# Performance work log

Hardware: AMD Instinct MI355X
Metric: run time of the kernel (lower is better)

## Reference

```python
import jax, jax.numpy as jnp
import numpy as np

B, Hn, Wn, C, NH, WS, SR = 4, 64, 64, 256, 8, 3, 8
HD = C // NH
N = Hn * Wn
L = WS * WS
PH, PW = Hn // SR, Wn // SR
P = PH * PW
T = 4096  # cpb table length
NEG = -1e30

def _l2norm(x, axis=-1):
    return x / jnp.maximum(jnp.linalg.norm(x, axis=axis, keepdims=True), 1e-12)

def _unfold(x, ws):
    # x: (B, C, H, W) -> (B, C, ws*ws, H*W), torch F.unfold channel ordering (C major)
    p = ws // 2
    b, c, h, w = x.shape
    xp = jnp.pad(x, ((0, 0), (0, 0), (p, p), (p, p)))
    pats = jnp.stack([xp[:, :, i:i + h, j:j + w] for i in range(ws) for j in range(ws)], axis=2)
    return pats.reshape(b, c, ws * ws, h * w)

def setup_inputs():
    key = jax.random.key(0)
    ks = jax.random.split(key, 16)
    def w(k, shape, s=0.02):
        return jax.random.normal(k, shape, jnp.float32) * s
    # buffers derived from the window geometry (get_seqlen_and_mask)
    ones = np.ones((Hn, Wn), np.float32)
    pad = WS // 2
    op = np.pad(ones, pad)
    pats = np.stack([op[i:i + Hn, j:j + Wn] for i in range(WS) for j in range(WS)], -1).reshape(N, L)
    padding_mask = jnp.asarray(pats == 0)
    seq_length_scale = jnp.asarray(np.log(pats.sum(-1, keepdims=True) + P).astype(np.float32))
    temperature = jnp.log(jnp.expm1(jnp.ones((NH, 1, 1), jnp.float32) / 0.24))
    return dict(
        x=jax.random.normal(ks[0], (B, N, C), jnp.float32),
        relative_pos_index=jax.random.randint(ks[1], (N, P), 0, T),
        relative_coords_table=jax.random.uniform(ks[2], (T, 2), jnp.float32, -1.0, 1.0),
        q_w=w(ks[3], (C, C)), q_b=jnp.zeros((C,), jnp.float32),
        kv_w=w(ks[4], (2 * C, C)), kv_b=jnp.zeros((2 * C,), jnp.float32),
        temperature=temperature,
        query_embedding=w(ks[5], (NH, 1, HD)),
        proj_w=w(ks[6], (C, C)), proj_b=jnp.zeros((C,), jnp.float32),
        sr_w=w(ks[7], (C, C)), sr_b=jnp.zeros((C,), jnp.float32),
        norm_g=jnp.ones((C,), jnp.float32), norm_b=jnp.zeros((C,), jnp.float32),
        cpb1_w=w(ks[8], (512, 2)), cpb1_b=jnp.zeros((512,), jnp.float32),
        cpb2_w=w(ks[9], (NH, 512)), cpb2_b=jnp.zeros((NH,), jnp.float32),
        rpb_local=w(ks[10], (NH, L), 0.0004),
        learnable_tokens=w(ks[11], (NH, HD, L)),
        learnable_bias=jnp.zeros((NH, 1, L), jnp.float32),
        seq_length_scale=seq_length_scale,
        padding_mask=padding_mask,
        H=Hn, W=Wn,
    )

def _forward(x, q_w, q_b, kv_w, kv_b, temperature, query_embedding, proj_w, proj_b,
             sr_w, sr_b, norm_g, norm_b, cpb1_w, cpb1_b, cpb2_w, cpb2_b, rpb_local,
             learnable_tokens, learnable_bias, seq_length_scale, relative_coords_table,
             relative_pos_index, padding_mask, H, W):
    b, n, c = x.shape
    # normalized queries, scaled by learnable temperature and log-seqlen
    q = (x @ q_w.T + q_b).reshape(b, n, NH, HD).transpose(0, 2, 1, 3)  # (B,h,N,d)
    q_norm = _l2norm(q)
    q_scaled = (q_norm + query_embedding[None]) * jax.nn.softplus(temperature)[None] * seq_length_scale
    # --- local branch: sliding-window QK with RPB ---
    kv = x @ kv_w.T + kv_b  # (B,N,2C)
    k_loc = _l2norm((kv[..., :c]).reshape(b, n, NH, HD)).reshape(b, n, c)
    kv_img = jnp.concatenate([k_loc, kv[..., c:]], -1).transpose(0, 2, 1).reshape(b, 2 * c, H, W)
    pats = _unfold(kv_img, WS).reshape(b, 2 * NH, HD, L, n).transpose(0, 1, 4, 2, 3)  # (B,2h,N,d,L)
    k_loc, v_loc = pats[:, :NH], pats[:, NH:]
    attn_local = jnp.einsum('bhnd,bhndl->bhnl', q_scaled, k_loc) + rpb_local[None, :, None, :]
    attn_local = jnp.where(padding_mask[None, None], NEG, attn_local)
    # --- pooled branch ---
    x_img = x.transpose(0, 2, 1).reshape(b, c, H, W)
    x_sr = jax.nn.gelu(jnp.einsum('bchw,oc->bohw', x_img, sr_w) + sr_b[None, :, None, None], approximate=False)
    x_pool = x_sr.reshape(b, c, PH, SR, PW, SR).mean((3, 5)).reshape(b, c, P).transpose(0, 2, 1)  # (B,P,C)
    mu = x_pool.mean(-1, keepdims=True)
    var = x_pool.var(-1, keepdims=True)
    x_pool = (x_pool - mu) / jnp.sqrt(var + 1e-5) * norm_g + norm_b
    kv_pool = (x_pool @ kv_w.T + kv_b).reshape(b, P, 2 * NH, HD).transpose(0, 2, 1, 3)
    k_pool, v_pool = kv_pool[:, :NH], kv_pool[:, NH:]  # (B,h,P,d)
    cpb = jax.nn.relu(relative_coords_table @ cpb1_w.T + cpb1_b) @ cpb2_w.T + cpb2_b  # (T,h)
    pool_bias = cpb.T[:, relative_pos_index.reshape(-1)].reshape(NH, n, P)
    attn_pool = jnp.einsum('bhnd,bhpd->bhnp', q_scaled, _l2norm(k_pool)) + pool_bias[None]
    # --- joint softmax over local + pooled keys ---
    attn = jax.nn.softmax(jnp.concatenate([attn_local, attn_pool], -1), axis=-1)
    attn_local, attn_pool = attn[..., :L], attn[..., L:]
    a = jnp.einsum('bhnd,hdl->bhnl', q_norm, learnable_tokens) + learnable_bias[None] + attn_local
    x_local = jnp.einsum('bhnl,bhndl->bhnd', a, v_loc)
    x_pool_out = jnp.einsum('bhnp,bhpd->bhnd', attn_pool, v_pool)
    out = (x_local + x_pool_out).transpose(0, 2, 1, 3).reshape(b, n, c)
    return out @ proj_w.T + proj_b

def reference(x, relative_pos_index, relative_coords_table, q_w, q_b, kv_w, kv_b, temperature,
              query_embedding, proj_w, proj_b, sr_w, sr_b, norm_g, norm_b, cpb1_w, cpb1_b,
              cpb2_w, cpb2_b, rpb_local, learnable_tokens, learnable_bias, seq_length_scale,
              padding_mask, H, W):
    return _forward(x, q_w, q_b, kv_w, kv_b, temperature, query_embedding, proj_w, proj_b,
                    sr_w, sr_b, norm_g, norm_b, cpb1_w, cpb1_b, cpb2_w, cpb2_b, rpb_local,
                    learnable_tokens, learnable_bias, seq_length_scale, relative_coords_table,
                    relative_pos_index, padding_mask, H, W)
```

## Files before the change

kernel.cpp:

```cpp
#include <hip/hip_runtime.h>
#include <hip/hip_bf16.h>

typedef unsigned short u16;
typedef unsigned int u32;

#define B_ 4
#define N_ 4096
#define C_ 256
#define NH_ 8
#define HD_ 32
#define L_ 9
#define P_ 64
#define T_ 4096
#define NEG_ (-1e30f)

typedef __attribute__((ext_vector_type(8))) short bf16x8;
typedef __attribute__((ext_vector_type(4))) float f32x4;

__device__ __forceinline__ float b2f(u16 u) {
    union { u32 i; float f; } v; v.i = ((u32)u) << 16; return v.f;
}
__device__ __forceinline__ u16 f2b(float f) {
    u32 x = __float_as_uint(f);
    u32 r = (x + 0x7fffu + ((x >> 16) & 1u)) >> 16;
    return (u16)r;
}
__device__ __forceinline__ short f2bs(float f) { return (short)f2b(f); }
__device__ __forceinline__ u32 cvtpk(float a, float b) {
    u32 r; asm("v_cvt_pk_bf16_f32 %0, %1, %2" : "=v"(r) : "v"(a), "v"(b)); return r;
}
union U8 { u32 u[4]; bf16x8 v; };

__global__ __launch_bounds__(256) void prep_k(
    const float* __restrict__ x, const float* __restrict__ q_w, const float* __restrict__ kv_w,
    const float* __restrict__ sr_w, const float* __restrict__ proj_w,
    u16* __restrict__ xb, u16* __restrict__ wfused, u16* __restrict__ pwb,
    const float* __restrict__ table, const float* __restrict__ w1, const float* __restrict__ b1,
    const float* __restrict__ w2, const float* __restrict__ b2, float* __restrict__ cpb)
{
    __shared__ float w1s[512][2];
    __shared__ float b1s[512];
    __shared__ float w2s[8][512];
    int bid = blockIdx.x, tid = threadIdx.x;
    if (bid < 4096) {
        int i = bid * 256 + tid;
        float4 v = reinterpret_cast<const float4*>(x)[i];
        ushort4 o; o.x = f2b(v.x); o.y = f2b(v.y); o.z = f2b(v.z); o.w = f2b(v.w);
        reinterpret_cast<ushort4*>(xb)[i] = o;
    } else if (bid < 4416) {
        int i = (bid - 4096) * 256 + tid;
        const float* s; u16* d; int off;
        if (i < 16384)      { s = q_w;    d = wfused; off = i; }
        else if (i < 49152) { s = kv_w;   d = wfused; off = i; }
        else if (i < 65536) { s = sr_w;   d = wfused; off = i; }
        else                { s = proj_w; d = pwb;    off = i - 65536; }
        int soff = (i < 16384) ? i : (i < 49152) ? (i - 16384) : (i < 65536) ? (i - 49152) : (i - 65536);
        float4 v = reinterpret_cast<const float4*>(s)[soff];
        ushort4 o; o.x = f2b(v.x); o.y = f2b(v.y); o.z = f2b(v.z); o.w = f2b(v.w);
        reinterpret_cast<ushort4*>(d)[off] = o;
    } else {
        for (int i = tid; i < 512; i += 256) {
            w1s[i][0] = w1[i * 2]; w1s[i][1] = w1[i * 2 + 1]; b1s[i] = b1[i];
        }
        for (int i = tid; i < 4096; i += 256) w2s[i >> 9][i & 511] = w2[i];
        __syncthreads();
        int t = (bid - 4416) * 256 + tid;
        float t0 = table[t * 2], t1 = table[t * 2 + 1];
        float acc[8] = {};
        for (int j = 0; j < 512; ++j) {
            float h = fmaxf(t0 * w1s[j][0] + t1 * w1s[j][1] + b1s[j], 0.0f);
            #pragma unroll
            for (int hh = 0; hh < 8; ++hh) acc[hh] += h * w2s[hh][j];
        }
        #pragma unroll
        for (int hh = 0; hh < 8; ++hh) cpb[t * 8 + hh] = acc[hh] + b2[hh];
    }
}

template<int MODE>
__global__ __launch_bounds__(256) void gemm_big_k(
    const u16* __restrict__ A, const u16* __restrict__ W,
    const float* __restrict__ b0, const float* __restrict__ b1, const float* __restrict__ b2,
    float* __restrict__ kvk, u16* __restrict__ kvv, u16* __restrict__ xgb, float* __restrict__ pout)
{
    constexpr int RI = (MODE == 0) ? 4 : 1;
    __shared__ u16 Bs[64 * 264];
    int tid = threadIdx.x, w = tid >> 6, lane = tid & 63;
    int quad = lane >> 4, l16 = lane & 15;
    int bx, by;
    {
        int i = blockIdx.x;
        if (MODE == 0) { bx = (i >> 3) % 12; by = (i & 7) + (i / 96) * 8; }
        else           { bx = (i >> 3) & 3;  by = (i & 7) + (i / 32) * 8; }
    }
    int colBase = (MODE == 0 ? 256 : 0) + bx * 64;
    #pragma unroll
    for (int c = 0; c < 8; ++c) {
        int linear = c * 256 + tid;
        int col = linear >> 5, kc = linear & 31;
        uint4 v = *reinterpret_cast<const uint4*>(W + (size_t)(colBase + col) * 256 + kc * 8);
        *reinterpret_cast<uint4*>(&Bs[col * 264 + kc * 8]) = v;
    }
    __syncthreads();
    int rowBase = by * (RI * 64) + w * (RI * 16);
    f32x4 acc[RI][4] = {};
    const u16* aptr = A + (size_t)(rowBase + l16) * 256 + quad * 8;
    bf16x8 afc[RI];
    #pragma unroll
    for (int i = 0; i < RI; ++i) afc[i] = *reinterpret_cast<const bf16x8*>(aptr + (size_t)i * 16 * 256);
    #pragma unroll
    for (int k0 = 0; k0 < 256; k0 += 32) {
        bf16x8 afn[RI];
        if (k0 < 224) {
            #pragma unroll
            for (int i = 0; i < RI; ++i)
                afn[i] = *reinterpret_cast<const bf16x8*>(aptr + (size_t)i * 16 * 256 + k0 + 32);
        }
        #pragma unroll
        for (int j = 0; j < 4; ++j) {
            bf16x8 bfr = *reinterpret_cast<const bf16x8*>(&Bs[(j * 16 + l16) * 264 + k0 + quad * 8]);
            #pragma unroll
            for (int i = 0; i < RI; ++i)
                acc[i][j] = __builtin_amdgcn_mfma_f32_16x16x32_bf16(afc[i], bfr, acc[i][j], 0, 0, 0);
        }
        if (k0 < 224) {
            #pragma unroll
            for (int i = 0; i < RI; ++i) afc[i] = afn[i];
        }
    }
    int rng = (MODE == 0) ? (colBase >> 8) : 99;
    float bj[4];
    #pragma unroll
    for (int j = 0; j < 4; ++j) {
        int gc = colBase + j * 16 + l16;
        if (MODE == 1)      bj[j] = b0[gc];
        else if (rng <= 2)  bj[j] = b1[gc - 256];
        else                bj[j] = b2[gc - 768];
    }
    #pragma unroll
    for (int i = 0; i < RI; ++i) {
        float vals[4][4];
        #pragma unroll
        for (int j = 0; j < 4; ++j)
            #pragma unroll
            for (int r = 0; r < 4; ++r) {
                float t = acc[i][j][r] + bj[j];
                if (MODE == 0 && rng == 3) t = 0.5f * t * (1.0f + erff(t * 0.70710678118654752f));
                vals[j][r] = t;
            }
        if (MODE == 0 && rng == 1) {
            #pragma unroll
            for (int hp = 0; hp < 2; ++hp)
                #pragma unroll
                for (int r = 0; r < 4; ++r) {
                    float s = vals[2*hp][r] * vals[2*hp][r] + vals[2*hp+1][r] * vals[2*hp+1][r];
                    s += __shfl_xor(s, 1); s += __shfl_xor(s, 2);
                    s += __shfl_xor(s, 4); s += __shfl_xor(s, 8);
                    float inv = 1.0f / fmaxf(sqrtf(s), 1e-12f);
                    vals[2*hp][r] *= inv; vals[2*hp+1][r] *= inv;
                }
        }
        #pragma unroll
        for (int j = 0; j < 4; ++j) {
            int gc = colBase + j * 16 + l16;
            #pragma unroll
            for (int r = 0; r < 4; ++r) {
                int row = rowBase + i * 16 + quad * 4 + r;
                if (MODE == 1)      pout[(size_t)row * 256 + gc] = vals[j][r];
                else if (rng == 1)  kvk[(size_t)row * 256 + gc - 256] = vals[j][r];
                else if (rng == 2)  kvv[(size_t)row * 256 + gc - 512] = f2b(vals[j][r]);
                else                xgb[(size_t)row * 256 + gc - 768] = f2b(vals[j][r]);
            }
        }
    }
}

__global__ __launch_bounds__(256) void poolkv_k(
    const u16* __restrict__ xgb, const float* __restrict__ g, const float* __restrict__ bta,
    const float* __restrict__ kv_w, const float* __restrict__ kv_b, float* __restrict__ kvp,
    const int* __restrict__ rpi, const float* __restrict__ cpb, float* __restrict__ biasp)
{
    int bid = blockIdx.x;
    int tid = threadIdx.x;
    if (bid >= 512) {
        int i = (bid - 512) * 256 + tid;
        int e0 = i * 4;
        int p = e0 & 63;
        int hn = e0 >> 6;
        int n = hn & 4095, h = hn >> 12;
        int4 idx4 = *reinterpret_cast<const int4*>(rpi + n * 64 + p);
        float4 o;
        o.x = cpb[(size_t)idx4.x * 8 + h];
        o.y = cpb[(size_t)idx4.y * 8 + h];
        o.z = cpb[(size_t)idx4.z * 8 + h];
        o.w = cpb[(size_t)idx4.w * 8 + h];
        *reinterpret_cast<float4*>(biasp + e0) = o;
        return;
    }
    __shared__ __align__(16) float xps[256];
    __shared__ float r1[4], r2[4];
    int bp = bid >> 1, half = bid & 1;
    int b = bp >> 6, p = bp & 63;
    int py = p >> 3, px = p & 7;
    int o = tid;
    float s = 0.0f;
    for (int sy = 0; sy < 8; ++sy)
        #pragma unroll
        for (int sx = 0; sx < 8; ++sx) {
            int pix = (py * 8 + sy) * 64 + px * 8 + sx;
            s += b2f(xgb[((size_t)(b * N_ + pix)) * C_ + o]);
        }
    float v = s * (1.0f / 64.0f);
    float s1 = v, s2 = v * v;
    #pragma unroll
    for (int off = 32; off >= 1; off >>= 1) { s1 += __shfl_xor(s1, off); s2 += __shfl_xor(s2, off); }
    int wv = o >> 6, ln = o & 63;
    if (ln == 0) { r1[wv] = s1; r2[wv] = s2; }
    __syncthreads();
    float S1 = r1[0] + r1[1] + r1[2] + r1[3];
    float S2 = r2[0] + r2[1] + r2[2] + r2[3];
    float mu = S1 * (1.0f / 256.0f);
    float var = S2 * (1.0f / 256.0f) - mu * mu;
    xps[o] = (v - mu) * rsqrtf(var + 1e-5f) * g[o] + bta[o];
    __syncthreads();
    int col = half * 256 + o;
    float a = kv_b[col];
    const float4* xp4 = (const float4*)xps;
    const float4* wrow = (const float4*)(kv_w + (size_t)col * 256);
    #pragma unroll 8
    for (int k4 = 0; k4 < 64; ++k4) {
        float4 xv = xp4[k4]; float4 wa = wrow[k4];
        a += xv.x * wa.x + xv.y * wa.y + xv.z * wa.z + xv.w * wa.w;
    }
    if (half == 0) {
        float ss = a * a;
        ss += __shfl_xor(ss, 1); ss += __shfl_xor(ss, 2); ss += __shfl_xor(ss, 4);
        ss += __shfl_xor(ss, 8); ss += __shfl_xor(ss, 16);
        a *= 1.0f / fmaxf(sqrtf(ss), 1e-12f);
    }
    kvp[(size_t)bp * 512 + col] = a;
}

__global__ __launch_bounds__(256) void attn_k(
    const u16* __restrict__ xb, const u16* __restrict__ qwb, const float* __restrict__ q_b,
    const float* __restrict__ kvk, const u16* __restrict__ kvv,
    const float* __restrict__ kvp, const float* __restrict__ biasp,
    const float* __restrict__ temp, const float* __restrict__ qe, const float* __restrict__ lt,
    const float* __restrict__ rpb, const float* __restrict__ lb,
    const float* __restrict__ slsin, u16* __restrict__ aob)
{
    __shared__ u16 kp_hi[64 * 40], kp_lo[64 * 40];
    __shared__ u16 vp_hi[32 * 72];
    __shared__ u16 ltb[16 * 32];
    __shared__ float S_w[4][16][76];
    __shared__ float rpb_s[9], lb_s[9];

    int bid = blockIdx.x;
    int tq = bid & 31, h = (bid >> 5) & 7, b = bid >> 8;
    int tid = threadIdx.x, wave = tid >> 6, lane = tid & 63;
    int quad = lane >> 4, l16 = lane & 15;

    {
        int p = tid >> 2, dc = (tid & 3) * 8;
        const float* src = kvp + ((size_t)(b * P_ + p)) * 512 + h * 32 + dc;
        float4 k0 = *(const float4*)(src), k1 = *(const float4*)(src + 4);
        float4 v0 = *(const float4*)(src + 256), v1 = *(const float4*)(src + 260);
        float kf[8] = {k0.x,k0.y,k0.z,k0.w,k1.x,k1.y,k1.z,k1.w};
        float vf[8] = {v0.x,v0.y,v0.z,v0.w,v1.x,v1.y,v1.z,v1.w};
        #pragma unroll
        for (int j2 = 0; j2 < 4; ++j2) {
            float a = kf[2*j2], c = kf[2*j2+1];
            u32 pk = cvtpk(a, c);
            *(u32*)&kp_hi[p * 40 + dc + 2*j2] = pk;
            float ra = __uint_as_float(pk << 16);
            float rb = __uint_as_float(pk & 0xffff0000u);
            *(u32*)&kp_lo[p * 40 + dc + 2*j2] = cvtpk(a - ra, c - rb);
            vp_hi[(dc + 2*j2) * 72 + p]     = f2b(vf[2*j2]);
            vp_hi[(dc + 2*j2 + 1) * 72 + p] = f2b(vf[2*j2+1]);
        }
    }
    for (int t = tid; t < 512; t += 256) {
        int l = t & 15, d = t >> 4;
        ltb[l * 32 + d] = (l < 9) ? f2b(lt[h * 288 + d * 9 + l]) : (u16)0;
    }
    if (tid < 9) { rpb_s[tid] = rpb[h * 9 + tid]; lb_s[tid] = lb[h * 9 + tid]; }
    float tsc = log1pf(expf(temp[h]));
    __syncthreads();

    const float* bp_h = biasp + (size_t)h * N_ * 64;

    #pragma unroll 1
    for (int it = 0; it < 2; ++it) {
        int tile = tq * 2 + it;
        int n0w = tile * 64 + wave * 16;
        int y = tile;

        f32x4 qacc[2] = {};
        {
            const u16* xrow = xb + ((size_t)(b * N_ + n0w + l16)) * 256 + quad * 8;
            const u16* qwr  = qwb + ((size_t)(h * 32 + l16)) * 256 + quad * 8;
            #pragma unroll
            for (int k0 = 0; k0 < 256; k0 += 32) {
                bf16x8 ax = *(const bf16x8*)(xrow + k0);
                bf16x8 bw0 = *(const bf16x8*)(qwr + k0);
                bf16x8 bw1 = *(const bf16x8*)(qwr + 16 * 256 + k0);
                qacc[0] = __builtin_amdgcn_mfma_f32_16x16x32_bf16(ax, bw0, qacc[0], 0, 0, 0);
                qacc[1] = __builtin_amdgcn_mfma_f32_16x16x32_bf16(ax, bw1, qacc[1], 0, 0, 0);
            }
        }
        {
            float qb0 = q_b[h * 32 + l16], qb1 = q_b[h * 32 + 16 + l16];
            float qe0 = qe[h * 32 + l16],  qe1 = qe[h * 32 + 16 + l16];
            #pragma unroll
            for (int r = 0; r < 4; ++r) {
                int p = quad * 4 + r;
                float v0 = qacc[0][r] + qb0, v1 = qacc[1][r] + qb1;
                float s = v0 * v0 + v1 * v1;
                s += __shfl_xor(s, 1); s += __shfl_xor(s, 2);
                s += __shfl_xor(s, 4); s += __shfl_xor(s, 8);
                float inv = 1.0f / fmaxf(sqrtf(s), 1e-12f);
                v0 *= inv; v1 *= inv;
                float sc = tsc * slsin[n0w + p];
                S_w[wave][p][40 + l16]      = (v0 + qe0) * sc;
                S_w[wave][p][40 + 16 + l16] = (v1 + qe1) * sc;
            }
        }
        bf16x8 qs_hi, qs_lo, qn_b;
        float qsr[8];
        {
            *(float4*)&qsr[0] = *(const float4*)&S_w[wave][l16][40 + quad * 8];
            *(float4*)&qsr[4] = *(const float4*)&S_w[wave][l16][40 + quad * 8 + 4];
            float invs = 1.0f / (tsc * slsin[n0w + l16]);
            const float* qep = qe + h * 32 + quad * 8;
            float4 e0 = *(const float4*)qep, e1 = *(const float4*)(qep + 4);
            float ef[8] = {e0.x,e0.y,e0.z,e0.w,e1.x,e1.y,e1.z,e1.w};
            U8 hiu, lou;
            #pragma unroll
            for (int j2 = 0; j2 < 4; ++j2) {
                float a = qsr[2*j2], c = qsr[2*j2+1];
                u32 pk = cvtpk(a, c);
                hiu.u[j2] = pk;
                float ra = __uint_as_float(pk << 16);
                float rb = __uint_as_float(pk & 0xffff0000u);
                lou.u[j2] = cvtpk(a - ra, c - rb);
            }
            qs_hi = hiu.v; qs_lo = lou.v;
            #pragma unroll
            for (int j = 0; j < 8; ++j)
                qn_b[j] = f2bs(qsr[j] * invs - ef[j]);
        }
        __builtin_amdgcn_s_setprio(1);
        #pragma unroll
        for (int jt = 0; jt < 4; ++jt) {
            bf16x8 bh = *(const bf16x8*)&kp_hi[(jt * 16 + l16) * 40 + quad * 8];
            bf16x8 bl = *(const bf16x8*)&kp_lo[(jt * 16 + l16) * 40 + quad * 8];
            f32x4 a = {};
            a = __builtin_amdgcn_mfma_f32_16x16x32_bf16(qs_lo, bh, a, 0, 0, 0);
            a = __builtin_amdgcn_mfma_f32_16x16x32_bf16(qs_hi, bl, a, 0, 0, 0);
            a = __builtin_amdgcn_mfma_f32_16x16x32_bf16(qs_hi, bh, a, 0, 0, 0);
            #pragma unroll
            for (int r = 0; r < 4; ++r) {
                int pix = quad * 4 + r;
                int n = n0w + pix;
                S_w[wave][pix][jt * 16 + l16] = a[r] + bp_h[(size_t)n * 64 + jt * 16 + l16];
            }
        }
        __builtin_amdgcn_s_setprio(0);
        f32x4 accL;
        {
            bf16x8 ltf = *(const bf16x8*)&ltb[l16 * 32 + quad * 8];
            f32x4 z = {};
            accL = __builtin_amdgcn_mfma_f32_16x16x32_bf16(qn_b, ltf, z, 0, 0, 0);
        }
        #pragma unroll
        for (int l = 0; l < 9; ++l) {
            int n = n0w + l16, x = n & 63;
            int ny = y + l / 3 - 1, nx = x + (l % 3) - 1;
            bool ok = ((unsigned)ny < 64u) && ((unsigned)nx < 64u);
            int nn = ok ? ny * 64 + nx : n;
            const float4* kb = (const float4*)(kvk + ((size_t)(b * N_ + nn)) * 256 + h * 32 + quad * 8);
            float4 k0v = kb[0], k1v = kb[1];
            float part = qsr[0]*k0v.x + qsr[1]*k0v.y + qsr[2]*k0v.z + qsr[3]*k0v.w
                       + qsr[4]*k1v.x + qsr[5]*k1v.y + qsr[6]*k1v.z + qsr[7]*k1v.w;
            part += __shfl_xor(part, 16);
            part += __shfl_xor(part, 32);
            if (quad == 0) S_w[wave][l16][64 + l] = ok ? (part + rpb_s[l]) : NEG_;
        }
        if (quad == 0) { S_w[wave][l16][73] = NEG_; S_w[wave][l16][74] = NEG_; S_w[wave][l16][75] = NEG_; }
        {
            int pix = lane >> 2, c0 = (lane & 3) * 19;
            float vals[19]; float mx = NEG_;
            #pragma unroll
            for (int i = 0; i < 19; ++i) { vals[i] = S_w[wave][pix][c0 + i]; mx = fmaxf(mx, vals[i]); }
            mx = fmaxf(mx, __shfl_xor(mx, 1));
            mx = fmaxf(mx, __shfl_xor(mx, 2));
            float sm = 0.0f;
            #pragma unroll
            for (int i = 0; i < 19; ++i) { vals[i] = __expf(vals[i] - mx); sm += vals[i]; }
            sm += __shfl_xor(sm, 1); sm += __shfl_xor(sm, 2);
            float inv = 1.0f / sm;
            #pragma unroll
            for (int i = 0; i < 19; ++i) S_w[wave][pix][c0 + i] = vals[i] * inv;
        }
        if (l16 < 9) {
            #pragma unroll
            for (int r = 0; r < 4; ++r) {
                int pix = quad * 4 + r;
                int n = n0w + pix, x = n & 63;
                int ny = y + l16 / 3 - 1, nx = x + (l16 % 3) - 1;
                bool ok = ((unsigned)ny < 64u) && ((unsigned)nx < 64u);
                float prev = S_w[wave][pix][64 + l16];
                S_w[wave][pix][64 + l16] = ok ? (accL[r] + lb_s[l16] + prev) : 0.0f;
            }
        }
        f32x4 accO[2] = {};
        __builtin_amdgcn_s_setprio(1);
        #pragma unroll
        for (int kc = 0; kc < 2; ++kc) {
            float wf[8];
            *(float4*)&wf[0] = *(const float4*)&S_w[wave][l16][kc * 32 + quad * 8];
            *(float4*)&wf[4] = *(const float4*)&S_w[wave][l16][kc * 32 + quad * 8 + 4];
            U8 hiu, lou;
            #pragma unroll
            for (int j2 = 0; j2 < 4; ++j2) {
                float a = wf[2*j2], c = wf[2*j2+1];
                u32 pk = cvtpk(a, c);
                hiu.u[j2] = pk;
                float ra = __uint_as_float(pk << 16);
                float rb = __uint_as_float(pk & 0xffff0000u);
                lou.u[j2] = cvtpk(a - ra, c - rb);
            }
            bf16x8 w_hi = hiu.v, w_lo = lou.v;
            #pragma unroll
            for (int nt = 0; nt < 2; ++nt) {
                bf16x8 vh = *(const bf16x8*)&vp_hi[(nt * 16 + l16) * 72 + kc * 32 + quad * 8];
                accO[nt] = __builtin_amdgcn_mfma_f32_16x16x32_bf16(w_lo, vh, accO[nt], 0, 0, 0);
                accO[nt] = __builtin_amdgcn_mfma_f32_16x16x32_bf16(w_hi, vh, accO[nt], 0, 0, 0);
            }
        }
        __builtin_amdgcn_s_setprio(0);
        {
            int xq0 = wave * 16 + quad * 4;
            #pragma unroll
            for (int dy = -1; dy <= 1; ++dy) {
                int ny = y + dy;
                bool rowOK = ((unsigned)ny < 64u);
                #pragma unroll
                for (int c = 0; c < 6; ++c) {
                    int xc = xq0 - 1 + c;
                    bool ok = rowOK && ((unsigned)xc < 64u);
                    int nn = ok ? ny * 64 + xc : 0;
                    const u16* vb = kvv + ((size_t)(b * N_ + nn)) * 256 + h * 32;
                    float v0 = b2f(vb[l16]);
                    float v1 = b2f(vb[16 + l16]);
                    #pragma unroll
                    for (int r = 0; r < 4; ++r) {
                        int dxr = c - 1 - r;
                        if (dxr >= -1 && dxr <= 1) {
                            int l = (dy + 1) * 3 + dxr + 1;
                            float aw = S_w[wave][quad * 4 + r][64 + l];
                            accO[0][r] += aw * v0;
                            accO[1][r] += aw * v1;
                        }
                    }
                }
            }
        }
        #pragma unroll
        for (int nt = 0; nt < 2; ++nt)
            #pragma unroll
            for (int r = 0; r < 4; ++r) {
                int n = n0w + quad * 4 + r;
                aob[((size_t)(b * N_ + n)) * C_ + h * 32 + nt * 16 + l16] = f2b(accO[nt][r]);
            }
    }
}

extern "C" void kernel_launch(void* const* d_in, const int* in_sizes, int n_in,
                              void* d_out, int out_size, void* d_ws, size_t ws_size,
                              hipStream_t stream) {
    const float* x      = (const float*)d_in[0];
    const int*   rpi    = (const int*)d_in[1];
    const float* table  = (const float*)d_in[2];
    const float* q_w    = (const float*)d_in[3];
    const float* q_b    = (const float*)d_in[4];
    const float* kv_w   = (const float*)d_in[5];
    const float* kv_b   = (const float*)d_in[6];
    const float* temp   = (const float*)d_in[7];
    const float* qe     = (const float*)d_in[8];
    const float* proj_w = (const float*)d_in[9];
    const float* proj_b = (const float*)d_in[10];
    const float* sr_w   = (const float*)d_in[11];
    const float* sr_b   = (const float*)d_in[12];
    const float* norm_g = (const float*)d_in[13];
    const float* norm_b = (const float*)d_in[14];
    const float* cpb1_w = (const float*)d_in[15];
    const float* cpb1_b = (const float*)d_in[16];
    const float* cpb2_w = (const float*)d_in[17];
    const float* cpb2_b = (const float*)d_in[18];
    const float* rpb    = (const float*)d_in[19];
    const float* lt     = (const float*)d_in[20];
    const float* lb     = (const float*)d_in[21];
    const float* sls    = (const float*)d_in[22];

    float* ws   = (float*)d_ws;
    float* kvk  = ws;
    float* kvp  = kvk + (size_t)B_ * N_ * C_;
    float* cpb  = kvp + (size_t)B_ * P_ * 2 * C_;
    float* bia  = cpb + (size_t)T_ * NH_;
    u16*   xb   = (u16*)(bia + (size_t)NH_ * N_ * P_);
    u16*   wfb  = xb  + (size_t)B_ * N_ * C_;
    u16*   pwb  = wfb + (size_t)1024 * C_;
    u16*   kvv  = pwb + (size_t)C_ * C_;
    u16*   xgb  = kvv + (size_t)B_ * N_ * C_;
    u16*   aob  = xgb;

    dim3 blk(256);

    prep_k<<<dim3(4432), blk, 0, stream>>>(x, q_w, kv_w, sr_w, proj_w, xb, wfb, pwb,
                                           table, cpb1_w, cpb1_b, cpb2_w, cpb2_b, cpb);
    gemm_big_k<0><<<dim3(768), blk, 0, stream>>>(xb, wfb, nullptr, kv_b, sr_b, kvk, kvv, xgb, nullptr);
    poolkv_k<<<dim3(2560), blk, 0, stream>>>(xgb, norm_g, norm_b, kv_w, kv_b, kvp, rpi, cpb, bia);
    attn_k<<<dim3(B_ * NH_ * 32), blk, 0, stream>>>(xb, wfb, q_b, kvk, kvv, kvp, bia,
                                                    temp, qe, lt, rpb, lb, sls, aob);
    gemm_big_k<1><<<dim3(1024), blk, 0, stream>>>(aob, pwb, proj_b, nullptr, nullptr,
                                                  nullptr, nullptr, nullptr, (float*)d_out);
}
```

Measured before the change: 257.2 us.

## Fuse CPB bias gather into attention via per-head LDS table

```diff
diff --git a/kernel.cpp b/kernel.cpp
--- a/kernel.cpp
+++ b/kernel.cpp
@@ -73,7 +73,7 @@
             for (int hh = 0; hh < 8; ++hh) acc[hh] += h * w2s[hh][j];
         }
         #pragma unroll
-        for (int hh = 0; hh < 8; ++hh) cpb[t * 8 + hh] = acc[hh] + b2[hh];
+        for (int hh = 0; hh < 8; ++hh) cpb[hh * 4096 + t] = acc[hh] + b2[hh];
     }
 }
 
@@ -177,26 +177,10 @@
 
 __global__ __launch_bounds__(256) void poolkv_k(
     const u16* __restrict__ xgb, const float* __restrict__ g, const float* __restrict__ bta,
-    const float* __restrict__ kv_w, const float* __restrict__ kv_b, float* __restrict__ kvp,
-    const int* __restrict__ rpi, const float* __restrict__ cpb, float* __restrict__ biasp)
+    const float* __restrict__ kv_w, const float* __restrict__ kv_b, float* __restrict__ kvp)
 {
     int bid = blockIdx.x;
     int tid = threadIdx.x;
-    if (bid >= 512) {
-        int i = (bid - 512) * 256 + tid;
-        int e0 = i * 4;
-        int p = e0 & 63;
-        int hn = e0 >> 6;
-        int n = hn & 4095, h = hn >> 12;
-        int4 idx4 = *reinterpret_cast<const int4*>(rpi + n * 64 + p);
-        float4 o;
-        o.x = cpb[(size_t)idx4.x * 8 + h];
-        o.y = cpb[(size_t)idx4.y * 8 + h];
-        o.z = cpb[(size_t)idx4.z * 8 + h];
-        o.w = cpb[(size_t)idx4.w * 8 + h];
-        *reinterpret_cast<float4*>(biasp + e0) = o;
-        return;
-    }
     __shared__ __align__(16) float xps[256];
     __shared__ float r1[4], r2[4];
     int bp = bid >> 1, half = bid & 1;
@@ -244,7 +228,7 @@
 __global__ __launch_bounds__(256) void attn_k(
     const u16* __restrict__ xb, const u16* __restrict__ qwb, const float* __restrict__ q_b,
     const float* __restrict__ kvk, const u16* __restrict__ kvv,
-    const float* __restrict__ kvp, const float* __restrict__ biasp,
+    const float* __restrict__ kvp, const int* __restrict__ rpi, const float* __restrict__ cpbt,
     const float* __restrict__ temp, const float* __restrict__ qe, const float* __restrict__ lt,
     const float* __restrict__ rpb, const float* __restrict__ lb,
     const float* __restrict__ slsin, u16* __restrict__ aob)
@@ -253,6 +237,7 @@
     __shared__ u16 vp_hi[32 * 72];
     __shared__ u16 ltb[16 * 32];
     __shared__ float S_w[4][16][76];
+    __shared__ __align__(16) float cpb_s[4096];
     __shared__ float rpb_s[9], lb_s[9];
 
     int bid = blockIdx.x;
@@ -279,6 +264,12 @@
             vp_hi[(dc + 2*j2 + 1) * 72 + p] = f2b(vf[2*j2+1]);
         }
     }
+    {
+        const float4* cp4 = (const float4*)(cpbt + (size_t)h * 4096);
+        float4* ds4 = (float4*)cpb_s;
+        #pragma unroll
+        for (int i = 0; i < 4; ++i) ds4[i * 256 + tid] = cp4[i * 256 + tid];
+    }
     for (int t = tid; t < 512; t += 256) {
         int l = t & 15, d = t >> 4;
         ltb[l * 32 + d] = (l < 9) ? f2b(lt[h * 288 + d * 9 + l]) : (u16)0;
@@ -286,8 +277,6 @@
     if (tid < 9) { rpb_s[tid] = rpb[h * 9 + tid]; lb_s[tid] = lb[h * 9 + tid]; }
     float tsc = log1pf(expf(temp[h]));
     __syncthreads();
-
-    const float* bp_h = biasp + (size_t)h * N_ * 64;
 
     #pragma unroll 1
     for (int it = 0; it < 2; ++it) {
@@ -358,11 +347,14 @@
             a = __builtin_amdgcn_mfma_f32_16x16x32_bf16(qs_lo, bh, a, 0, 0, 0);
             a = __builtin_amdgcn_mfma_f32_16x16x32_bf16(qs_hi, bl, a, 0, 0, 0);
             a = __builtin_amdgcn_mfma_f32_16x16x32_bf16(qs_hi, bh, a, 0, 0, 0);
+            int idx[4];
+            #pragma unroll
+            for (int r = 0; r < 4; ++r)
+                idx[r] = rpi[(size_t)(n0w + quad * 4 + r) * 64 + jt * 16 + l16];
             #pragma unroll
             for (int r = 0; r < 4; ++r) {
                 int pix = quad * 4 + r;
-                int n = n0w + pix;
-                S_w[wave][pix][jt * 16 + l16] = a[r] + bp_h[(size_t)n * 64 + jt * 16 + l16];
+                S_w[wave][pix][jt * 16 + l16] = a[r] + cpb_s[idx[r]];
             }
         }
         __builtin_amdgcn_s_setprio(0);
@@ -507,8 +499,7 @@
     float* kvk  = ws;
     float* kvp  = kvk + (size_t)B_ * N_ * C_;
     float* cpb  = kvp + (size_t)B_ * P_ * 2 * C_;
-    float* bia  = cpb + (size_t)T_ * NH_;
-    u16*   xb   = (u16*)(bia + (size_t)NH_ * N_ * P_);
+    u16*   xb   = (u16*)(cpb + (size_t)T_ * NH_);
     u16*   wfb  = xb  + (size_t)B_ * N_ * C_;
     u16*   pwb  = wfb + (size_t)1024 * C_;
     u16*   kvv  = pwb + (size_t)C_ * C_;
@@ -520,8 +511,8 @@
     prep_k<<<dim3(4432), blk, 0, stream>>>(x, q_w, kv_w, sr_w, proj_w, xb, wfb, pwb,
                                            table, cpb1_w, cpb1_b, cpb2_w, cpb2_b, cpb);
     gemm_big_k<0><<<dim3(768), blk, 0, stream>>>(xb, wfb, nullptr, kv_b, sr_b, kvk, kvv, xgb, nullptr);
-    poolkv_k<<<dim3(2560), blk, 0, stream>>>(xgb, norm_g, norm_b, kv_w, kv_b, kvp, rpi, cpb, bia);
-    attn_k<<<dim3(B_ * NH_ * 32), blk, 0, stream>>>(xb, wfb, q_b, kvk, kvv, kvp, bia,
+    poolkv_k<<<dim3(512), blk, 0, stream>>>(xgb, norm_g, norm_b, kv_w, kv_b, kvp);
+    attn_k<<<dim3(B_ * NH_ * 32), blk, 0, stream>>>(xb, wfb, q_b, kvk, kvv, kvp, rpi, cpb,
                                                     temp, qe, lt, rpb, lb, sls, aob);
     gemm_big_k<1><<<dim3(1024), blk, 0, stream>>>(aob, pwb, proj_b, nullptr, nullptr,
                                                   nullptr, nullptr, nullptr, (float*)d_out);
```

New measurement: 243.2 us. -5.4%, faster.
